# Optimization experiments

Measured on AMD Instinct MI355X. Metric: run time of the kernel, lower is better.

## Reference

```python
import jax, jax.numpy as jnp
import numpy as np

DIM = 1024
HEADS = 16
DIM_HEAD = 64
INNER = HEADS * DIM_HEAD  # 1024
N = 1024  # seq len == n_features
B = 8
EPS = 1e-5


def setup_inputs() -> dict:
    key = jax.random.key(0)
    ks = jax.random.split(key, 6)
    x = jax.random.normal(ks[0], (B, N, DIM), dtype=jnp.float32)
    ln_gamma = jnp.ones((DIM,), dtype=jnp.float32)
    ln_beta = jnp.zeros((DIM,), dtype=jnp.float32)
    # torch Linear weight is [out, in]; we store transposed [in, out] for x @ W
    w_qkv = jax.random.normal(ks[1], (DIM, 3 * INNER), dtype=jnp.float32) * (DIM ** -0.5)
    w_out = jax.random.normal(ks[2], (INNER, DIM), dtype=jnp.float32) * (INNER ** -0.5)
    attn_bias = jax.random.normal(ks[3], (1, HEADS, N, N), dtype=jnp.float32) * 0.02
    return {"x": x, "ln_gamma": ln_gamma, "ln_beta": ln_beta,
            "w_qkv": w_qkv, "w_out": w_out, "attn_bias": attn_bias}


def reference(x, ln_gamma, ln_beta, w_qkv, w_out, attn_bias):
    # LayerNorm over last dim
    mu = jnp.mean(x, axis=-1, keepdims=True)
    var = jnp.var(x, axis=-1, keepdims=True)
    xn = (x - mu) * jax.lax.rsqrt(var + EPS) * ln_gamma + ln_beta
    # QKV projection (no bias)
    qkv = xn @ w_qkv  # [b, n, 3*inner]
    q, k, v = jnp.split(qkv, 3, axis=-1)
    def to_heads(t):
        return t.reshape(B, N, HEADS, DIM_HEAD).transpose(0, 2, 1, 3)  # b h n d
    q, k, v = to_heads(q), to_heads(k), to_heads(v)
    scale = DIM_HEAD ** -0.5
    q = q * scale
    sim = jnp.einsum('bhid,bhjd->bhij', q, k) + attn_bias  # [b,h,n,n]
    attn = jax.nn.softmax(sim, axis=-1)
    # dropout p=0.0 -> identity
    out = jnp.einsum('bhij,bhjd->bhid', attn, v)  # [b,h,n,d]
    out = out.transpose(0, 2, 1, 3).reshape(B, N, INNER)  # b n (h d)
    return out @ w_out
```

## Files before the change

### kernel.cpp

```cpp
#include <hip/hip_runtime.h>


#define DIM    1024
#define HEADS  16
#define DHEAD  64
#define INNER  1024
#define SEQ    1024
#define BATCH  8
#define QKV3   3072

typedef __bf16 bf16x8 __attribute__((ext_vector_type(8)));
typedef float f32x4 __attribute__((ext_vector_type(4)));
typedef unsigned short u16x8 __attribute__((ext_vector_type(8)));
typedef unsigned short u16x4 __attribute__((ext_vector_type(4)));

typedef __attribute__((address_space(1))) const unsigned int as1_uint;
typedef __attribute__((address_space(3))) unsigned int as3_uint;

static __device__ inline unsigned short f2bf(float f) {
  unsigned int u = __float_as_uint(f);
  u = (u + 0x7FFFu + ((u >> 16) & 1u)) >> 16;
  return (unsigned short)u;
}
static __device__ inline unsigned short f2bf_fast(float f) {
  __bf16 h = (__bf16)f;
  return __builtin_bit_cast(unsigned short, h);
}

__global__ __launch_bounds__(256) void ln_bf16_kernel(
    const float* __restrict__ x, const float* __restrict__ gamma,
    const float* __restrict__ beta, unsigned short* __restrict__ xn) {
  int row = blockIdx.x;
  int tid = threadIdx.x;
  const float4* xr = reinterpret_cast<const float4*>(x + (size_t)row * DIM);
  float4 v = xr[tid];
  float s = v.x + v.y + v.z + v.w;
  float s2 = v.x * v.x + v.y * v.y + v.z * v.z + v.w * v.w;
#pragma unroll
  for (int m = 32; m; m >>= 1) {
    s += __shfl_xor(s, m, 64);
    s2 += __shfl_xor(s2, m, 64);
  }
  __shared__ float red[2][4];
  int wid = tid >> 6, lane = tid & 63;
  if (lane == 0) { red[0][wid] = s; red[1][wid] = s2; }
  __syncthreads();
  s = red[0][0] + red[0][1] + red[0][2] + red[0][3];
  s2 = red[1][0] + red[1][1] + red[1][2] + red[1][3];
  float mu = s * (1.0f / DIM);
  float var = s2 * (1.0f / DIM) - mu * mu;
  float rstd = rsqrtf(var + 1e-5f);
  float4 g = reinterpret_cast<const float4*>(gamma)[tid];
  float4 b = reinterpret_cast<const float4*>(beta)[tid];
  u16x4 o;
  o[0] = f2bf((v.x - mu) * rstd * g.x + b.x);
  o[1] = f2bf((v.y - mu) * rstd * g.y + b.y);
  o[2] = f2bf((v.z - mu) * rstd * g.z + b.z);
  o[3] = f2bf((v.w - mu) * rstd * g.w + b.w);
  *reinterpret_cast<u16x4*>(xn + (size_t)row * DIM + tid * 4) = o;
}

__global__ __launch_bounds__(256) void transpose_cvt(
    const float* __restrict__ W, unsigned short* __restrict__ Wt, int R, int C,
    int scale_rows) {
  __shared__ float tb[32][33];
  int c0 = blockIdx.x * 32, r0 = blockIdx.y * 32;
  int tx = threadIdx.x, ty = threadIdx.y;
#pragma unroll
  for (int i = 0; i < 4; ++i)
    tb[ty + i * 8][tx] = W[(size_t)(r0 + ty + i * 8) * C + c0 + tx];
  __syncthreads();
#pragma unroll
  for (int i = 0; i < 4; ++i) {
    int orow = c0 + ty + i * 8;
    float v = tb[tx][ty + i * 8];
    if (orow < scale_rows) v *= 0.125f;
    Wt[(size_t)orow * R + r0 + tx] = f2bf(v);
  }
}

template <bool F32OUT>
__global__ __launch_bounds__(256) void gemm_bt(
    const unsigned short* __restrict__ A, const unsigned short* __restrict__ Bt,
    void* __restrict__ Cout, int M, int N, int K) {
  __shared__ unsigned short As[128 * 64];
  __shared__ unsigned short Bs[128 * 64];
  int nb = N >> 7;
  int bm = blockIdx.x / nb, bn = blockIdx.x % nb;
  int tid = threadIdx.x, wid = tid >> 6, lane = tid & 63;
  int wr = wid >> 1, wc = wid & 1;
  int lg = lane >> 4, lr = lane & 15;
  f32x4 acc[4][4] = {};
  const unsigned short* Ablk = A + (size_t)(bm * 128) * K;
  const unsigned short* Bblk = Bt + (size_t)(bn * 128) * K;
  int srow = wid * 32 + (lane >> 3);
  int scol = (lane & 7) * 8;
  for (int kt = 0; kt < K; kt += 64) {
#pragma unroll
    for (int t = 0; t < 4; ++t) {
      int r = srow + t * 8;
      __builtin_amdgcn_global_load_lds(
          (as1_uint*)(Ablk + (size_t)r * K + kt + scol),
          (as3_uint*)(&As[(wid * 32 + t * 8) * 64]), 16, 0, 0);
      __builtin_amdgcn_global_load_lds(
          (as1_uint*)(Bblk + (size_t)r * K + kt + scol),
          (as3_uint*)(&Bs[(wid * 32 + t * 8) * 64]), 16, 0, 0);
    }
    __syncthreads();
#pragma unroll
    for (int kk = 0; kk < 2; ++kk) {
      bf16x8 af[4], bfr[4];
#pragma unroll
      for (int mi = 0; mi < 4; ++mi)
        af[mi] = *reinterpret_cast<const bf16x8*>(
            &As[(wr * 64 + mi * 16 + lr) * 64 + kk * 32 + lg * 8]);
#pragma unroll
      for (int ni = 0; ni < 4; ++ni)
        bfr[ni] = *reinterpret_cast<const bf16x8*>(
            &Bs[(wc * 64 + ni * 16 + lr) * 64 + kk * 32 + lg * 8]);
#pragma unroll
      for (int mi = 0; mi < 4; ++mi)
#pragma unroll
        for (int ni = 0; ni < 4; ++ni)
          acc[mi][ni] = __builtin_amdgcn_mfma_f32_16x16x32_bf16(
              af[mi], bfr[ni], acc[mi][ni], 0, 0, 0);
    }
    __syncthreads();
  }
#pragma unroll
  for (int mi = 0; mi < 4; ++mi) {
    int row = bm * 128 + wr * 64 + mi * 16 + lg * 4;
#pragma unroll
    for (int ni = 0; ni < 4; ++ni) {
      int col = bn * 128 + wc * 64 + ni * 16 + lr;
#pragma unroll
      for (int j = 0; j < 4; ++j) {
        if (F32OUT)
          ((float*)Cout)[(size_t)(row + j) * N + col] = acc[mi][ni][j];
        else
          ((unsigned short*)Cout)[(size_t)(row + j) * N + col] = f2bf(acc[mi][ni][j]);
      }
    }
  }
}

__global__ __launch_bounds__(256) void attn_kernel(
    const unsigned short* __restrict__ qkv, const float* __restrict__ bias,
    unsigned short* __restrict__ aout) {
  int phys = blockIdx.x;
  int id = (phys & 7) * 128 + (phys >> 3);
  int b = id & 7, qt = (id >> 3) & 7, h = id >> 6;
  int tid = threadIdx.x, wid = tid >> 6, lane = tid & 63;
  int lg = lane >> 4, lr = lane & 15;

  __shared__ unsigned short Ks[2][64 * 64];
  __shared__ unsigned short Vt[2][64 * 72];
  __shared__ unsigned short Ps[4][32 * 72];

  const unsigned short* qbase = qkv + (size_t)(b * SEQ) * QKV3 + h * 64;
  const unsigned short* kbase = qbase + INNER;
  const unsigned short* vbase = qbase + 2 * INNER;
  const float* biash = bias + (size_t)h * SEQ * SEQ;

  int q0 = qt * 128 + wid * 32;

  bf16x8 qf[2][2];
#pragma unroll
  for (int mi = 0; mi < 2; ++mi)
#pragma unroll
    for (int kk = 0; kk < 2; ++kk)
      qf[mi][kk] = *reinterpret_cast<const bf16x8*>(
          qbase + (size_t)(q0 + mi * 16 + lr) * QKV3 + kk * 32 + lg * 8);

  const float* brow[2];
#pragma unroll
  for (int mi = 0; mi < 2; ++mi)
    brow[mi] = biash + (size_t)(q0 + mi * 16 + lr) * SEQ;

  int vrow = tid & 63;
  int vchunk = tid >> 6;
  int krow_in = lane >> 3;
  int kchunk = lane & 7;
  int kxor = lr & 7;

#pragma unroll
  for (int i = 0; i < 2; ++i) {
    int r = wid * 16 + i * 8 + krow_in;
    __builtin_amdgcn_global_load_lds(
        (as1_uint*)(kbase + (size_t)r * QKV3 + (kchunk ^ (r & 7)) * 8),
        (as3_uint*)(&Ks[0][(wid * 16 + i * 8) * 64]), 16, 0, 0);
  }
  u16x8 vreg[2];
#pragma unroll
  for (int it = 0; it < 2; ++it)
    vreg[it] = *reinterpret_cast<const u16x8*>(
        vbase + (size_t)vrow * QKV3 + (vchunk + it * 4) * 8);

  f32x4 oacc[2][4] = {};
  float mrun[2] = {-1e30f, -1e30f}, lrun[2] = {0.f, 0.f};

#define ATTN_STEP(TT, BUF, PREFETCH)                                           \
  {                                                                            \
    _Pragma("unroll") for (int it = 0; it < 2; ++it)                           \
        _Pragma("unroll") for (int i = 0; i < 8; ++i)                          \
            Vt[BUF][((vchunk + it * 4) * 8 + i) * 72 + vrow] = vreg[it][i];    \
    __syncthreads();                                                           \
    if (PREFETCH) {                                                            \
      _Pragma("unroll") for (int i = 0; i < 2; ++i) {                          \
        int r = wid * 16 + i * 8 + krow_in;                                    \
        __builtin_amdgcn_global_load_lds(                                      \
            (as1_uint*)(kbase + (size_t)(((TT) + 1) * 64 + r) * QKV3 +         \
                        (kchunk ^ (r & 7)) * 8),                               \
            (as3_uint*)(&Ks[1 - (BUF)][(wid * 16 + i * 8) * 64]), 16, 0, 0);   \
      }                                                                        \
      _Pragma("unroll") for (int it = 0; it < 2; ++it)                         \
          vreg[it] = *reinterpret_cast<const u16x8*>(                          \
              vbase + (size_t)(((TT) + 1) * 64 + vrow) * QKV3 +                \
              (vchunk + it * 4) * 8);                                          \
    }                                                                          \
    f32x4 bv[2][4];                                                            \
    _Pragma("unroll") for (int mi = 0; mi < 2; ++mi)                           \
        _Pragma("unroll") for (int kb = 0; kb < 4; ++kb)                       \
            bv[mi][kb] = *reinterpret_cast<const f32x4*>(                      \
                brow[mi] + (TT) * 64 + kb * 16 + lg * 4);                      \
    f32x4 s[2][4] = {};                                                        \
    const unsigned short* ksb = Ks[BUF];                                       \
    __builtin_amdgcn_s_setprio(1);                                             \
    _Pragma("unroll") for (int kb = 0; kb < 4; ++kb) {                         \
      int rowb = (kb * 16 + lr) * 64;                                          \
      bf16x8 k0 = *reinterpret_cast<const bf16x8*>(                            \
          ksb + rowb + ((lg ^ kxor) << 3));                                    \
      bf16x8 k1 = *reinterpret_cast<const bf16x8*>(                            \
          ksb + rowb + (((4 + lg) ^ kxor) << 3));                              \
      _Pragma("unroll") for (int mi = 0; mi < 2; ++mi) {                       \
        s[mi][kb] = __builtin_amdgcn_mfma_f32_16x16x32_bf16(                   \
            k0, qf[mi][0], s[mi][kb], 0, 0, 0);                                \
        s[mi][kb] = __builtin_amdgcn_mfma_f32_16x16x32_bf16(                   \
            k1, qf[mi][1], s[mi][kb], 0, 0, 0);                                \
      }                                                                        \
    }                                                                          \
    __builtin_amdgcn_s_setprio(0);                                             \
    _Pragma("unroll") for (int mi = 0; mi < 2; ++mi)                           \
        _Pragma("unroll") for (int kb = 0; kb < 4; ++kb)                       \
            _Pragma("unroll") for (int j = 0; j < 4; ++j)                      \
                s[mi][kb][j] += bv[mi][kb][j];                                 \
    float alpha[2];                                                            \
    _Pragma("unroll") for (int mi = 0; mi < 2; ++mi) {                         \
      float t0 = fmaxf(fmaxf(s[mi][0][0], s[mi][0][1]),                        \
                       fmaxf(s[mi][0][2], s[mi][0][3]));                       \
      float t1 = fmaxf(fmaxf(s[mi][1][0], s[mi][1][1]),                        \
                       fmaxf(s[mi][1][2], s[mi][1][3]));                       \
      float t2 = fmaxf(fmaxf(s[mi][2][0], s[mi][2][1]),                        \
                       fmaxf(s[mi][2][2], s[mi][2][3]));                       \
      float t3 = fmaxf(fmaxf(s[mi][3][0], s[mi][3][1]),                        \
                       fmaxf(s[mi][3][2], s[mi][3][3]));                       \
      float rm = fmaxf(fmaxf(t0, t1), fmaxf(t2, t3));                          \
      rm = fmaxf(rm, __shfl_xor(rm, 16, 64));                                  \
      rm = fmaxf(rm, __shfl_xor(rm, 32, 64));                                  \
      float mnew = fmaxf(mrun[mi], rm);                                        \
      alpha[mi] = __expf(mrun[mi] - mnew);                                     \
      mrun[mi] = mnew;                                                         \
      float ls = 0.f;                                                          \
      _Pragma("unroll") for (int kb = 0; kb < 4; ++kb) {                       \
        float e0 = __expf(s[mi][kb][0] - mnew);                                \
        float e1 = __expf(s[mi][kb][1] - mnew);                                \
        float e2 = __expf(s[mi][kb][2] - mnew);                                \
        float e3 = __expf(s[mi][kb][3] - mnew);                                \
        s[mi][kb][0] = e0; s[mi][kb][1] = e1;                                  \
        s[mi][kb][2] = e2; s[mi][kb][3] = e3;                                  \
        ls += (e0 + e1) + (e2 + e3);                                           \
      }                                                                        \
      ls += __shfl_xor(ls, 16, 64);                                            \
      ls += __shfl_xor(ls, 32, 64);                                            \
      lrun[mi] = lrun[mi] * alpha[mi] + ls;                                    \
    }                                                                          \
    _Pragma("unroll") for (int mi = 0; mi < 2; ++mi)                           \
        _Pragma("unroll") for (int kb = 0; kb < 4; ++kb) {                     \
      u16x4 pk;                                                                \
      pk[0] = f2bf_fast(s[mi][kb][0]);                                         \
      pk[1] = f2bf_fast(s[mi][kb][1]);                                         \
      pk[2] = f2bf_fast(s[mi][kb][2]);                                         \
      pk[3] = f2bf_fast(s[mi][kb][3]);                                         \
      *reinterpret_cast<u16x4*>(                                               \
          &Ps[wid][(mi * 16 + lr) * 72 + kb * 16 + lg * 4]) = pk;              \
    }                                                                          \
    asm volatile("s_waitcnt lgkmcnt(0)" ::: "memory");                         \
    __builtin_amdgcn_sched_barrier(0);                                         \
    _Pragma("unroll") for (int mi = 0; mi < 2; ++mi)                           \
        _Pragma("unroll") for (int db = 0; db < 4; ++db)                       \
            _Pragma("unroll") for (int j = 0; j < 4; ++j)                      \
                oacc[mi][db][j] *= alpha[mi];                                  \
    __builtin_amdgcn_s_setprio(1);                                             \
    _Pragma("unroll") for (int k2 = 0; k2 < 2; ++k2) {                         \
      bf16x8 va[4], pb[2];                                                     \
      _Pragma("unroll") for (int db = 0; db < 4; ++db)                         \
          va[db] = *reinterpret_cast<const bf16x8*>(                           \
              &Vt[BUF][(db * 16 + lr) * 72 + k2 * 32 + lg * 8]);               \
      _Pragma("unroll") for (int mi = 0; mi < 2; ++mi)                         \
          pb[mi] = *reinterpret_cast<const bf16x8*>(                           \
              &Ps[wid][(mi * 16 + lr) * 72 + k2 * 32 + lg * 8]);               \
      _Pragma("unroll") for (int mi = 0; mi < 2; ++mi)                         \
          _Pragma("unroll") for (int db = 0; db < 4; ++db)                     \
              oacc[mi][db] = __builtin_amdgcn_mfma_f32_16x16x32_bf16(          \
                  va[db], pb[mi], oacc[mi][db], 0, 0, 0);                      \
    }                                                                          \
    __builtin_amdgcn_s_setprio(0);                                             \
  }

  for (int t = 0; t < 16; t += 2) {
    ATTN_STEP(t, 0, true);
    ATTN_STEP(t + 1, 1, (t + 1) < 15);
  }
#undef ATTN_STEP

#pragma unroll
  for (int mi = 0; mi < 2; ++mi) {
    float inv = 1.0f / lrun[mi];
    size_t row = (size_t)(b * SEQ + q0 + mi * 16 + lr) * INNER + h * 64;
#pragma unroll
    for (int db = 0; db < 4; ++db) {
      u16x4 o;
      o[0] = f2bf_fast(oacc[mi][db][0] * inv);
      o[1] = f2bf_fast(oacc[mi][db][1] * inv);
      o[2] = f2bf_fast(oacc[mi][db][2] * inv);
      o[3] = f2bf_fast(oacc[mi][db][3] * inv);
      *reinterpret_cast<u16x4*>(&aout[row + db * 16 + lg * 4]) = o;
    }
  }
}

extern "C" void kernel_launch(void* const* d_in, const int* in_sizes, int n_in,
                              void* d_out, int out_size, void* d_ws, size_t ws_size,
                              hipStream_t stream) {
  const float* x = (const float*)d_in[0];
  const float* gamma = (const float*)d_in[1];
  const float* beta = (const float*)d_in[2];
  const float* w_qkv = (const float*)d_in[3];
  const float* w_out = (const float*)d_in[4];
  const float* bias = (const float*)d_in[5];

  char* ws = (char*)d_ws;
  unsigned short* xn = (unsigned short*)(ws);
  unsigned short* wqkv_t = (unsigned short*)(ws + 16777216);
  unsigned short* wout_t = (unsigned short*)(ws + 23068672);
  unsigned short* qkvb = (unsigned short*)(ws + 25165824);
  unsigned short* aout = (unsigned short*)(ws + 75497472);

  ln_bf16_kernel<<<BATCH * SEQ, 256, 0, stream>>>(x, gamma, beta, xn);
  transpose_cvt<<<dim3(QKV3 / 32, DIM / 32), dim3(32, 8), 0, stream>>>(
      w_qkv, wqkv_t, DIM, QKV3, INNER);
  transpose_cvt<<<dim3(DIM / 32, INNER / 32), dim3(32, 8), 0, stream>>>(
      w_out, wout_t, INNER, DIM, 0);
  gemm_bt<false><<<(BATCH * SEQ / 128) * (QKV3 / 128), 256, 0, stream>>>(
      xn, wqkv_t, (void*)qkvb, BATCH * SEQ, QKV3, DIM);
  attn_kernel<<<BATCH * HEADS * (SEQ / 128), 256, 0, stream>>>(qkvb, bias, aout);
  gemm_bt<true><<<(BATCH * SEQ / 128) * (DIM / 128), 256, 0, stream>>>(
      aout, wout_t, d_out, BATCH * SEQ, DIM, INNER);
}
```

Measured before the change: 349.9 us.

## Pipeline GEMM with triple-buffered LDS ring, swizzled layout and XCD block remap

Replaces the single-buffered GEMM, which synchronised twice per K step, with a three-stage LDS ring of 32-wide K tiles. Global-to-LDS loads for tile k+2 are issued before the MFMAs on tile k, with one barrier per step gated on vmcnt. The LDS layout XOR-swizzles 8-element column chunks to cut bank conflicts, and block IDs are remapped across the 8 XCDs to improve L2 locality. The ring wraps its load index modulo NT, so the last two iterations issue redundant loads, and the vmcnt-based waits assume a fixed count of outstanding loads per stage.

New measurement: 335.8 us. 1.04x faster.

```diff
diff --git a/kernel.cpp b/kernel.cpp
--- a/kernel.cpp
+++ b/kernel.cpp
@@ -80,53 +80,91 @@
 }
 
 template <bool F32OUT>
-__global__ __launch_bounds__(256) void gemm_bt(
+__global__ __launch_bounds__(256) void gemm_ring(
     const unsigned short* __restrict__ A, const unsigned short* __restrict__ Bt,
     void* __restrict__ Cout, int M, int N, int K) {
-  __shared__ unsigned short As[128 * 64];
-  __shared__ unsigned short Bs[128 * 64];
+  __shared__ unsigned short As[3][128 * 32];
+  __shared__ unsigned short Bs[3][128 * 32];
   int nb = N >> 7;
-  int bm = blockIdx.x / nb, bn = blockIdx.x % nb;
+  int nwg = (M >> 7) * nb;
+  int cpx = nwg >> 3;
+  int phys = blockIdx.x;
+  int swz = (phys & 7) * cpx + (phys >> 3);
+  int bm = swz / nb, bn = swz % nb;
   int tid = threadIdx.x, wid = tid >> 6, lane = tid & 63;
   int wr = wid >> 1, wc = wid & 1;
   int lg = lane >> 4, lr = lane & 15;
-  f32x4 acc[4][4] = {};
   const unsigned short* Ablk = A + (size_t)(bm * 128) * K;
   const unsigned short* Bblk = Bt + (size_t)(bn * 128) * K;
-  int srow = wid * 32 + (lane >> 3);
-  int scol = (lane & 7) * 8;
-  for (int kt = 0; kt < K; kt += 64) {
-#pragma unroll
-    for (int t = 0; t < 4; ++t) {
-      int r = srow + t * 8;
-      __builtin_amdgcn_global_load_lds(
-          (as1_uint*)(Ablk + (size_t)r * K + kt + scol),
-          (as3_uint*)(&As[(wid * 32 + t * 8) * 64]), 16, 0, 0);
-      __builtin_amdgcn_global_load_lds(
-          (as1_uint*)(Bblk + (size_t)r * K + kt + scol),
-          (as3_uint*)(&Bs[(wid * 32 + t * 8) * 64]), 16, 0, 0);
-    }
-    __syncthreads();
-#pragma unroll
-    for (int kk = 0; kk < 2; ++kk) {
-      bf16x8 af[4], bfr[4];
-#pragma unroll
-      for (int mi = 0; mi < 4; ++mi)
-        af[mi] = *reinterpret_cast<const bf16x8*>(
-            &As[(wr * 64 + mi * 16 + lr) * 64 + kk * 32 + lg * 8]);
+
+  int sr0 = wid * 32 + (lane >> 2);
+  int sc = lane & 3;
+  int r0 = sr0, r1 = sr0 + 16;
+  size_t aoff0 = (size_t)r0 * K + (sc ^ ((r0 >> 1) & 3)) * 8;
+  size_t aoff1 = (size_t)r1 * K + (sc ^ ((r1 >> 1) & 3)) * 8;
+  int ldst0 = (wid * 32) * 32;
+  int ldst1 = (wid * 32 + 16) * 32;
+  int NT = K >> 5;
+
+  int rdc = (lg ^ ((lr >> 1) & 3)) * 8;
+
+  f32x4 acc[4][4] = {};
+
+#pragma unroll
+  for (int t2 = 0; t2 < 2; ++t2) {
+    __builtin_amdgcn_global_load_lds((as1_uint*)(Ablk + aoff0 + t2 * 32),
+                                     (as3_uint*)(&As[t2][ldst0]), 16, 0, 0);
+    __builtin_amdgcn_global_load_lds((as1_uint*)(Bblk + aoff0 + t2 * 32),
+                                     (as3_uint*)(&Bs[t2][ldst0]), 16, 0, 0);
+    __builtin_amdgcn_global_load_lds((as1_uint*)(Ablk + aoff1 + t2 * 32),
+                                     (as3_uint*)(&As[t2][ldst1]), 16, 0, 0);
+    __builtin_amdgcn_global_load_lds((as1_uint*)(Bblk + aoff1 + t2 * 32),
+                                     (as3_uint*)(&Bs[t2][ldst1]), 16, 0, 0);
+  }
+  asm volatile("s_waitcnt vmcnt(4)" ::: "memory");
+  __builtin_amdgcn_s_barrier();
+  asm volatile("" ::: "memory");
+
+  int s0 = 0;
+  for (int kt = 0; kt < NT; ++kt) {
+    const unsigned short* as = As[s0];
+    const unsigned short* bs = Bs[s0];
+    bf16x8 a[4], b[4];
+#pragma unroll
+    for (int mi = 0; mi < 4; ++mi)
+      a[mi] = *reinterpret_cast<const bf16x8*>(
+          as + (wr * 64 + mi * 16 + lr) * 32 + rdc);
+#pragma unroll
+    for (int ni = 0; ni < 4; ++ni)
+      b[ni] = *reinterpret_cast<const bf16x8*>(
+          bs + (wc * 64 + ni * 16 + lr) * 32 + rdc);
+
+    int st = kt + 2; if (st >= NT) st -= NT;
+    int ss = s0 + 2; if (ss >= 3) ss -= 3;
+    __builtin_amdgcn_global_load_lds((as1_uint*)(Ablk + aoff0 + st * 32),
+                                     (as3_uint*)(&As[ss][ldst0]), 16, 0, 0);
+    __builtin_amdgcn_global_load_lds((as1_uint*)(Bblk + aoff0 + st * 32),
+                                     (as3_uint*)(&Bs[ss][ldst0]), 16, 0, 0);
+    __builtin_amdgcn_global_load_lds((as1_uint*)(Ablk + aoff1 + st * 32),
+                                     (as3_uint*)(&As[ss][ldst1]), 16, 0, 0);
+    __builtin_amdgcn_global_load_lds((as1_uint*)(Bblk + aoff1 + st * 32),
+                                     (as3_uint*)(&Bs[ss][ldst1]), 16, 0, 0);
+
+    __builtin_amdgcn_s_setprio(1);
+#pragma unroll
+    for (int mi = 0; mi < 4; ++mi)
 #pragma unroll
       for (int ni = 0; ni < 4; ++ni)
-        bfr[ni] = *reinterpret_cast<const bf16x8*>(
-            &Bs[(wc * 64 + ni * 16 + lr) * 64 + kk * 32 + lg * 8]);
-#pragma unroll
-      for (int mi = 0; mi < 4; ++mi)
-#pragma unroll
-        for (int ni = 0; ni < 4; ++ni)
-          acc[mi][ni] = __builtin_amdgcn_mfma_f32_16x16x32_bf16(
-              af[mi], bfr[ni], acc[mi][ni], 0, 0, 0);
-    }
-    __syncthreads();
-  }
+        acc[mi][ni] = __builtin_amdgcn_mfma_f32_16x16x32_bf16(
+            a[mi], b[ni], acc[mi][ni], 0, 0, 0);
+    __builtin_amdgcn_s_setprio(0);
+
+    asm volatile("s_waitcnt vmcnt(4)" ::: "memory");
+    __builtin_amdgcn_s_barrier();
+    asm volatile("" ::: "memory");
+    s0 = (s0 == 2) ? 0 : s0 + 1;
+  }
+
 #pragma unroll
   for (int mi = 0; mi < 4; ++mi) {
     int row = bm * 128 + wr * 64 + mi * 16 + lg * 4;
@@ -351,9 +389,9 @@
       w_qkv, wqkv_t, DIM, QKV3, INNER);
   transpose_cvt<<<dim3(DIM / 32, INNER / 32), dim3(32, 8), 0, stream>>>(
       w_out, wout_t, INNER, DIM, 0);
-  gemm_bt<false><<<(BATCH * SEQ / 128) * (QKV3 / 128), 256, 0, stream>>>(
+  gemm_ring<false><<<(BATCH * SEQ / 128) * (QKV3 / 128), 256, 0, stream>>>(
       xn, wqkv_t, (void*)qkvb, BATCH * SEQ, QKV3, DIM);
   attn_kernel<<<BATCH * HEADS * (SEQ / 128), 256, 0, stream>>>(qkvb, bias, aout);
-  gemm_bt<true><<<(BATCH * SEQ / 128) * (DIM / 128), 256, 0, stream>>>(
+  gemm_ring<true><<<(BATCH * SEQ / 128) * (DIM / 128), 256, 0, stream>>>(
       aout, wout_t, d_out, BATCH * SEQ, DIM, INNER);
 }
```

## Replace GEMM with 256x256 tile, 8-wave, double-buffered ping-pong pipelined kernel

Applied to the files above, without the earlier changes.

Replaces the 128x128 single-buffered GEMM with a 256x256 tile kernel running 8 waves. It double-buffers LDS and splits each K-step into four phases that interleave global-to-LDS loads with MFMA bursts, using setprio and explicit barriers. It also adds an XOR swizzle on LDS chunks to avoid bank conflicts and an XCD-aware block remap. The goal is to hide memory latency and raise operand reuse in both projection GEMMs, at the cost of fewer workgroups (tail effects on the small output GEMM) and heavy register and LDS use.

Result: faster. 342.9 us (-2.0%).

```diff
diff --git a/kernel.cpp b/kernel.cpp
--- a/kernel.cpp
+++ b/kernel.cpp
@@ -80,59 +80,166 @@
 }
 
 template <bool F32OUT>
-__global__ __launch_bounds__(256) void gemm_bt(
+__global__ __launch_bounds__(512, 2) void gemm8(
     const unsigned short* __restrict__ A, const unsigned short* __restrict__ Bt,
     void* __restrict__ Cout, int M, int N, int K) {
-  __shared__ unsigned short As[128 * 64];
-  __shared__ unsigned short Bs[128 * 64];
-  int nb = N >> 7;
-  int bm = blockIdx.x / nb, bn = blockIdx.x % nb;
+  __shared__ unsigned short As[2][256 * 64];
+  __shared__ unsigned short Bs[2][256 * 64];
+  const int nb = N >> 8;
+  const int nwg = (M >> 8) * nb;
+  const int cpx = nwg >> 3;
+  int phys = blockIdx.x;
+  int swz = (phys & 7) * cpx + (phys >> 3);
+  int bm = swz / nb, bn = swz % nb;
   int tid = threadIdx.x, wid = tid >> 6, lane = tid & 63;
-  int wr = wid >> 1, wc = wid & 1;
+  int wr = wid >> 2, wc = wid & 3;
   int lg = lane >> 4, lr = lane & 15;
-  f32x4 acc[4][4] = {};
-  const unsigned short* Ablk = A + (size_t)(bm * 128) * K;
-  const unsigned short* Bblk = Bt + (size_t)(bn * 128) * K;
-  int srow = wid * 32 + (lane >> 3);
-  int scol = (lane & 7) * 8;
-  for (int kt = 0; kt < K; kt += 64) {
-#pragma unroll
-    for (int t = 0; t < 4; ++t) {
-      int r = srow + t * 8;
-      __builtin_amdgcn_global_load_lds(
-          (as1_uint*)(Ablk + (size_t)r * K + kt + scol),
-          (as3_uint*)(&As[(wid * 32 + t * 8) * 64]), 16, 0, 0);
-      __builtin_amdgcn_global_load_lds(
-          (as1_uint*)(Bblk + (size_t)r * K + kt + scol),
-          (as3_uint*)(&Bs[(wid * 32 + t * 8) * 64]), 16, 0, 0);
-    }
-    __syncthreads();
-#pragma unroll
-    for (int kk = 0; kk < 2; ++kk) {
-      bf16x8 af[4], bfr[4];
-#pragma unroll
-      for (int mi = 0; mi < 4; ++mi)
-        af[mi] = *reinterpret_cast<const bf16x8*>(
-            &As[(wr * 64 + mi * 16 + lr) * 64 + kk * 32 + lg * 8]);
-#pragma unroll
-      for (int ni = 0; ni < 4; ++ni)
-        bfr[ni] = *reinterpret_cast<const bf16x8*>(
-            &Bs[(wc * 64 + ni * 16 + lr) * 64 + kk * 32 + lg * 8]);
-#pragma unroll
-      for (int mi = 0; mi < 4; ++mi)
-#pragma unroll
-        for (int ni = 0; ni < 4; ++ni)
+  const unsigned short* Ablk = A + (size_t)(bm * 256) * K;
+  const unsigned short* Bblk = Bt + (size_t)(bn * 256) * K;
+  const int NT = K >> 6;
+
+  int srow8 = lane >> 3;
+  int schk = lane & 7;
+  int axr = lr & 7;
+
+#define G_STAGE_A(BUF, MH, KT)                                                 \
+  {                                                                            \
+    _Pragma("unroll") for (int i = 0; i < 2; ++i) {                            \
+      int rb = (MH) * 64 + i * 128 + (wid << 3);                               \
+      int r = rb + srow8;                                                      \
+      __builtin_amdgcn_global_load_lds(                                        \
+          (as1_uint*)(Ablk + (size_t)r * K + (KT) * 64 +                       \
+                      ((schk ^ (r & 7)) << 3)),                                \
+          (as3_uint*)(&As[BUF][rb * 64]), 16, 0, 0);                           \
+    }                                                                          \
+  }
+#define G_STAGE_B(BUF, NH, KT)                                                 \
+  {                                                                            \
+    _Pragma("unroll") for (int i = 0; i < 2; ++i) {                            \
+      int c = i * 8 + wid;                                                     \
+      int rb = ((c >> 2) << 6) + (NH) * 32 + ((c & 3) << 3);                   \
+      int r = rb + srow8;                                                      \
+      __builtin_amdgcn_global_load_lds(                                        \
+          (as1_uint*)(Bblk + (size_t)r * K + (KT) * 64 +                       \
+                      ((schk ^ (r & 7)) << 3)),                                \
+          (as3_uint*)(&Bs[BUF][rb * 64]), 16, 0, 0);                           \
+    }                                                                          \
+  }
+#define LDA(BUF, MI, KK)                                                       \
+  (*reinterpret_cast<const bf16x8*>(                                           \
+      &As[BUF][(wr * 128 + (MI) * 16 + lr) * 64 +                              \
+               ((((KK) * 4 + lg) ^ axr) << 3)]))
+#define LDB(BUF, NI, KK)                                                       \
+  (*reinterpret_cast<const bf16x8*>(                                           \
+      &Bs[BUF][(wc * 64 + (NI) * 16 + lr) * 64 +                               \
+               ((((KK) * 4 + lg) ^ axr) << 3)]))
+#define PHASE_SYNC_IN()                                                        \
+  asm volatile("" ::: "memory");                                               \
+  __builtin_amdgcn_s_barrier();                                                \
+  asm volatile("s_waitcnt lgkmcnt(0)" ::: "memory");                           \
+  __builtin_amdgcn_sched_barrier(0);                                           \
+  __builtin_amdgcn_s_setprio(1);
+#define PHASE_SYNC_OUT()                                                       \
+  __builtin_amdgcn_s_setprio(0);                                               \
+  __builtin_amdgcn_s_barrier();                                                \
+  asm volatile("" ::: "memory");
+
+  f32x4 acc[8][4] = {};
+  bf16x8 af[4][2], bfr[4][2];
+
+  G_STAGE_A(0, 0, 0);
+  G_STAGE_B(0, 0, 0);
+  G_STAGE_A(0, 1, 0);
+  G_STAGE_B(0, 1, 0);
+  if (NT > 1) {
+    G_STAGE_A(1, 0, 1);
+    G_STAGE_B(1, 0, 1);
+  }
+  asm volatile("s_waitcnt vmcnt(4)" ::: "memory");
+  __builtin_amdgcn_s_barrier();
+  asm volatile("" ::: "memory");
+
+  for (int t = 0; t < NT; ++t) {
+    int cur = t & 1, nxt = cur ^ 1;
+    int s1 = (t + 1 < NT) ? t + 1 : 0;
+    int s2 = (t + 2 < NT) ? t + 2 : t + 2 - NT;
+
+#pragma unroll
+    for (int mi = 0; mi < 4; ++mi)
+#pragma unroll
+      for (int kk = 0; kk < 2; ++kk) af[mi][kk] = LDA(cur, mi, kk);
+#pragma unroll
+    for (int ni = 0; ni < 2; ++ni)
+#pragma unroll
+      for (int kk = 0; kk < 2; ++kk) bfr[ni][kk] = LDB(cur, ni, kk);
+    G_STAGE_A(nxt, 1, s1);
+    PHASE_SYNC_IN();
+#pragma unroll
+    for (int mi = 0; mi < 4; ++mi)
+#pragma unroll
+      for (int ni = 0; ni < 2; ++ni)
+#pragma unroll
+        for (int kk = 0; kk < 2; ++kk)
           acc[mi][ni] = __builtin_amdgcn_mfma_f32_16x16x32_bf16(
-              af[mi], bfr[ni], acc[mi][ni], 0, 0, 0);
-    }
-    __syncthreads();
-  }
-#pragma unroll
-  for (int mi = 0; mi < 4; ++mi) {
-    int row = bm * 128 + wr * 64 + mi * 16 + lg * 4;
+              af[mi][kk], bfr[ni][kk], acc[mi][ni], 0, 0, 0);
+    PHASE_SYNC_OUT();
+
+#pragma unroll
+    for (int ni = 2; ni < 4; ++ni)
+#pragma unroll
+      for (int kk = 0; kk < 2; ++kk) bfr[ni][kk] = LDB(cur, ni, kk);
+    G_STAGE_B(nxt, 1, s1);
+    PHASE_SYNC_IN();
+#pragma unroll
+    for (int mi = 0; mi < 4; ++mi)
+#pragma unroll
+      for (int ni = 2; ni < 4; ++ni)
+#pragma unroll
+        for (int kk = 0; kk < 2; ++kk)
+          acc[mi][ni] = __builtin_amdgcn_mfma_f32_16x16x32_bf16(
+              af[mi][kk], bfr[ni][kk], acc[mi][ni], 0, 0, 0);
+    PHASE_SYNC_OUT();
+
+#pragma unroll
+    for (int mi = 0; mi < 4; ++mi)
+#pragma unroll
+      for (int kk = 0; kk < 2; ++kk) af[mi][kk] = LDA(cur, 4 + mi, kk);
+    G_STAGE_A(cur, 0, s2);
+    PHASE_SYNC_IN();
+#pragma unroll
+    for (int mi = 0; mi < 4; ++mi)
+#pragma unroll
+      for (int ni = 0; ni < 2; ++ni)
+#pragma unroll
+        for (int kk = 0; kk < 2; ++kk)
+          acc[4 + mi][ni] = __builtin_amdgcn_mfma_f32_16x16x32_bf16(
+              af[mi][kk], bfr[ni][kk], acc[4 + mi][ni], 0, 0, 0);
+    PHASE_SYNC_OUT();
+
+    G_STAGE_B(cur, 0, s2);
+    asm volatile("" ::: "memory");
+    __builtin_amdgcn_s_barrier();
+    __builtin_amdgcn_s_setprio(1);
+#pragma unroll
+    for (int mi = 0; mi < 4; ++mi)
+#pragma unroll
+      for (int ni = 2; ni < 4; ++ni)
+#pragma unroll
+        for (int kk = 0; kk < 2; ++kk)
+          acc[4 + mi][ni] = __builtin_amdgcn_mfma_f32_16x16x32_bf16(
+              af[mi][kk], bfr[ni][kk], acc[4 + mi][ni], 0, 0, 0);
+    __builtin_amdgcn_s_setprio(0);
+    asm volatile("s_waitcnt vmcnt(4)" ::: "memory");
+    __builtin_amdgcn_s_barrier();
+    asm volatile("" ::: "memory");
+  }
+
+#pragma unroll
+  for (int mi = 0; mi < 8; ++mi) {
+    int row = bm * 256 + wr * 128 + mi * 16 + lg * 4;
 #pragma unroll
     for (int ni = 0; ni < 4; ++ni) {
-      int col = bn * 128 + wc * 64 + ni * 16 + lr;
+      int col = bn * 256 + wc * 64 + ni * 16 + lr;
 #pragma unroll
       for (int j = 0; j < 4; ++j) {
         if (F32OUT)
@@ -142,6 +249,12 @@
       }
     }
   }
+#undef G_STAGE_A
+#undef G_STAGE_B
+#undef LDA
+#undef LDB
+#undef PHASE_SYNC_IN
+#undef PHASE_SYNC_OUT
 }
 
 __global__ __launch_bounds__(256) void attn_kernel(
@@ -351,9 +464,9 @@
       w_qkv, wqkv_t, DIM, QKV3, INNER);
   transpose_cvt<<<dim3(DIM / 32, INNER / 32), dim3(32, 8), 0, stream>>>(
       w_out, wout_t, INNER, DIM, 0);
-  gemm_bt<false><<<(BATCH * SEQ / 128) * (QKV3 / 128), 256, 0, stream>>>(
+  gemm8<false><<<(BATCH * SEQ / 256) * (QKV3 / 256), 512, 0, stream>>>(
       xn, wqkv_t, (void*)qkvb, BATCH * SEQ, QKV3, DIM);
   attn_kernel<<<BATCH * HEADS * (SEQ / 128), 256, 0, stream>>>(qkvb, bias, aout);
-  gemm_bt<true><<<(BATCH * SEQ / 128) * (DIM / 128), 256, 0, stream>>>(
+  gemm8<true><<<(BATCH * SEQ / 256) * (DIM / 256), 512, 0, stream>>>(
       aout, wout_t, d_out, BATCH * SEQ, DIM, INNER);
 }
```
